# Kernel tuning notes

Hardware: AMD Instinct MI355X
Metric: run time of the kernel (lower is better)

The kernel has to match this reference:

```python
import jax, jax.numpy as jnp
import numpy as np

D = 768
H = 12
B, T = 2, 2048


def _layernorm(x, g, b, eps=1e-5):
    m = jnp.mean(x, axis=-1, keepdims=True)
    v = jnp.mean((x - m) ** 2, axis=-1, keepdims=True)
    return (x - m) * jax.lax.rsqrt(v + eps) * g + b


def setup_inputs() -> dict:
    key = jax.random.key(0)
    ks = jax.random.split(key, 10)
    s = 0.02
    return {
        "x": jax.random.normal(ks[0], (B, T, D), dtype=jnp.float32),
        "attn_mask": jnp.ones((B, T), dtype=jnp.int32),
        "Wq": jax.random.normal(ks[1], (D, D), dtype=jnp.float32) * s,
        "Wk": jax.random.normal(ks[2], (D, D), dtype=jnp.float32) * s,
        "Wv": jax.random.normal(ks[3], (D, D), dtype=jnp.float32) * s,
        "Wo": jax.random.normal(ks[4], (D, D), dtype=jnp.float32) * s,
        "bo": jnp.zeros((D,), dtype=jnp.float32),
        "ln1_g": jnp.ones((D,), dtype=jnp.float32),
        "ln1_b": jnp.zeros((D,), dtype=jnp.float32),
        "ln2_g": jnp.ones((D,), dtype=jnp.float32),
        "ln2_b": jnp.zeros((D,), dtype=jnp.float32),
        "W1": jax.random.normal(ks[5], (D, 4 * D), dtype=jnp.float32) * s,
        "b1": jnp.zeros((4 * D,), dtype=jnp.float32),
        "W2": jax.random.normal(ks[6], (4 * D, D), dtype=jnp.float32) * s,
        "b2": jnp.zeros((D,), dtype=jnp.float32),
    }


def reference(x, attn_mask, Wq, Wk, Wv, Wo, bo, ln1_g, ln1_b, ln2_g, ln2_b, W1, b1, W2, b2):
    d = x.shape[-1]
    hs = d // H
    # --- multi-head self-attention on ln1(x) ---
    h = _layernorm(x, ln1_g, ln1_b)
    q = jnp.einsum("btd,dhk->bhtk", h, Wq.reshape(d, H, hs))
    k = jnp.einsum("btd,dhk->bhtk", h, Wk.reshape(d, H, hs))
    v = jnp.einsum("btd,dhk->bhtk", h, Wv.reshape(d, H, hs))
    # NOTE: original scales by embed_dim**-0.5 (C = embed_dim), not head_size
    scores = jnp.einsum("bhtk,bhsk->bhts", q, k) * (d ** -0.5)
    key_mask = (attn_mask == 0)[:, None, None, :]  # [B,1,1,T] over key dim
    scores = jnp.where(key_mask, -jnp.inf, scores)
    wei = jax.nn.softmax(scores, axis=-1)
    out = jnp.einsum("bhts,bhsk->bhtk", wei, v)
    out = out.transpose(0, 2, 1, 3).reshape(x.shape)  # concat heads -> [B,T,D]
    x = x + out @ Wo + bo
    # --- feed-forward on ln2(x) ---
    h2 = _layernorm(x, ln2_g, ln2_b)
    ff = jax.nn.relu(h2 @ W1 + b1) @ W2 + b2
    return x + ff
```

## Files before the change

kernel.cpp:

```cpp
#include <hip/hip_runtime.h>
#include <hip/hip_bf16.h>


typedef unsigned short u16;
typedef unsigned int u32;
typedef __attribute__((ext_vector_type(8))) short s16x8;
typedef __attribute__((ext_vector_type(4))) short s16x4;
typedef __attribute__((ext_vector_type(4))) float fx4;

#define D_MODEL 768
#define NH 12
#define HS 64
#define TT 2048
#define BB 2

__device__ __forceinline__ u16 f2bf(float f) {
  union { float f; u32 u; } v; v.f = f;
  u32 r = v.u + 0x7fffu + ((v.u >> 16) & 1u);
  return (u16)(r >> 16);
}
__device__ __forceinline__ float bf2f(u16 h) {
  union { u32 u; float f; } v; v.u = ((u32)h) << 16; return v.f;
}
__device__ __forceinline__ s16x4 pack4(float a, float b, float c, float d) {
  union { __hip_bfloat162 h2[2]; s16x4 v; } u;
  u.h2[0] = __float22bfloat162_rn({a, b});
  u.h2[1] = __float22bfloat162_rn({c, d});
  return u.v;
}

__device__ __forceinline__ void async16(const void* g, void* l) {
  __builtin_amdgcn_global_load_lds(
      (const __attribute__((address_space(1))) u32*)g,
      (__attribute__((address_space(3))) u32*)l, 16, 0, 0);
}

__global__ __launch_bounds__(256) void preproc(
    const float* __restrict__ x, const int* __restrict__ mask,
    const float* __restrict__ Wq, const float* __restrict__ Wk,
    const float* __restrict__ Wv, const float* __restrict__ Wo,
    const float* __restrict__ W1, const float* __restrict__ W2,
    const float* __restrict__ g1, const float* __restrict__ be1,
    u16* __restrict__ WqkvT, u16* __restrict__ WoT,
    u16* __restrict__ W1T, u16* __restrict__ W2T,
    u16* __restrict__ h1, float* __restrict__ mb) {
  __shared__ float t[32][33];
  __shared__ float ss[4], ssq[4];
  const int bid = blockIdx.x, tid = threadIdx.x;
  if (bid < 6912) {
    const float* in; u16* out; int R, C, cx, cy;
    if (bid < 1728) {
      int wsel = bid / 576, s = bid % 576;
      in = wsel == 0 ? Wq : wsel == 1 ? Wk : Wv;
      out = WqkvT + (size_t)wsel * 768 * 768;
      R = 768; C = 768; cx = s % 24; cy = s / 24;
    } else if (bid < 2304) {
      int s = bid - 1728; in = Wo; out = WoT;
      R = 768; C = 768; cx = s % 24; cy = s / 24;
    } else if (bid < 4608) {
      int s = bid - 2304; in = W1; out = W1T;
      R = 768; C = 3072; cx = s % 96; cy = s / 96;
    } else {
      int s = bid - 4608; in = W2; out = W2T;
      R = 3072; C = 768; cx = s % 24; cy = s / 24;
    }
    int c0 = cx * 32, r0 = cy * 32, xx = tid & 31, yy = tid >> 5;
    for (int i = 0; i < 4; i++)
      t[yy + i * 8][xx] = in[(size_t)(r0 + yy + i * 8) * C + c0 + xx];
    __syncthreads();
    for (int i = 0; i < 4; i++)
      out[(size_t)(c0 + yy + i * 8) * R + r0 + xx] = f2bf(t[xx][yy + i * 8]);
  } else if (bid < 11008) {
    int row = bid - 6912;
    const float* xr = x + (size_t)row * D_MODEL;
    float v0 = xr[tid], v1 = xr[tid + 256], v2 = xr[tid + 512];
    float s = v0 + v1 + v2, sq = v0 * v0 + v1 * v1 + v2 * v2;
    for (int m = 1; m < 64; m <<= 1) { s += __shfl_xor(s, m); sq += __shfl_xor(sq, m); }
    int w = tid >> 6;
    if ((tid & 63) == 0) { ss[w] = s; ssq[w] = sq; }
    __syncthreads();
    s = ss[0] + ss[1] + ss[2] + ss[3];
    sq = ssq[0] + ssq[1] + ssq[2] + ssq[3];
    float mean = s * (1.f / D_MODEL);
    float var = sq * (1.f / D_MODEL) - mean * mean;
    float rstd = rsqrtf(var + 1e-5f);
    u16* orow = h1 + (size_t)row * D_MODEL;
    orow[tid]       = f2bf((v0 - mean) * rstd * g1[tid]       + be1[tid]);
    orow[tid + 256] = f2bf((v1 - mean) * rstd * g1[tid + 256] + be1[tid + 256]);
    orow[tid + 512] = f2bf((v2 - mean) * rstd * g1[tid + 512] + be1[tid + 512]);
  } else {
    int i = (bid - 11008) * 256 + tid;
    mb[i] = mask[i] ? 0.f : -1e30f;
  }
}

__global__ __launch_bounds__(256) void red_wo_ln(
    const u16* __restrict__ p0, const u16* __restrict__ p1,
    const u16* __restrict__ p2, const u16* __restrict__ p3,
    const float* __restrict__ x, const float* __restrict__ bo,
    const float* __restrict__ g, const float* __restrict__ be,
    float* __restrict__ yv, u16* __restrict__ h2) {
  int row = blockIdx.x, tid = threadIdx.x;
  size_t base = (size_t)row * D_MODEL;
  float v[3];
  float s = 0.f, sq = 0.f;
  for (int i = 0; i < 3; i++) {
    int c = tid + i * 256;
    size_t idx = base + c;
    float t = bf2f(p0[idx]) + bf2f(p1[idx]) + bf2f(p2[idx]) + bf2f(p3[idx])
            + x[idx] + bo[c];
    v[i] = t; yv[idx] = t;
    s += t; sq += t * t;
  }
  for (int m = 1; m < 64; m <<= 1) { s += __shfl_xor(s, m); sq += __shfl_xor(sq, m); }
  __shared__ float ss[4], ssq[4];
  int w = tid >> 6;
  if ((tid & 63) == 0) { ss[w] = s; ssq[w] = sq; }
  __syncthreads();
  s = ss[0] + ss[1] + ss[2] + ss[3];
  sq = ssq[0] + ssq[1] + ssq[2] + ssq[3];
  float mean = s * (1.f / D_MODEL);
  float var = sq * (1.f / D_MODEL) - mean * mean;
  float rstd = rsqrtf(var + 1e-5f);
  for (int i = 0; i < 3; i++) {
    int c = tid + i * 256;
    h2[base + c] = f2bf((v[i] - mean) * rstd * g[c] + be[c]);
  }
}

__global__ __launch_bounds__(256) void red_ff2(
    const u16* __restrict__ p0, const u16* __restrict__ p1,
    const u16* __restrict__ p2, const float* __restrict__ yv,
    const float* __restrict__ bias, float* __restrict__ out) {
  size_t i = ((size_t)blockIdx.x * 256 + threadIdx.x) * 4;
  int col = (int)(i % D_MODEL);
  ushort4 a = *(const ushort4*)(p0 + i);
  ushort4 b = *(const ushort4*)(p1 + i);
  ushort4 c = *(const ushort4*)(p2 + i);
  float4 y = *(const float4*)(yv + i);
  float4 o;
  o.x = bf2f(a.x) + bf2f(b.x) + bf2f(c.x) + y.x + bias[col];
  o.y = bf2f(a.y) + bf2f(b.y) + bf2f(c.y) + y.y + bias[col + 1];
  o.z = bf2f(a.z) + bf2f(b.z) + bf2f(c.z) + y.z + bias[col + 2];
  o.w = bf2f(a.w) + bf2f(b.w) + bf2f(c.w) + y.w + bias[col + 3];
  *(float4*)(out + i) = o;
}

template <int EPI>
__global__ __launch_bounds__(256) void gemm_bt(
    const u16* __restrict__ A, const u16* __restrict__ Bt,
    int M, int N, int K,
    u16* __restrict__ outb, const float* __restrict__ bias,
    float qs, u16* __restrict__ vtp,
    u16* __restrict__ p0, u16* __restrict__ p1,
    u16* __restrict__ p2, u16* __restrict__ p3) {
  __shared__ __align__(16) u16 lA[128 * 64];
  __shared__ __align__(16) u16 lB[128 * 64];
  const int tid = threadIdx.x;
  const int lane = tid & 63, w = tid >> 6;
  const int quad = lane >> 4, l15 = lane & 15;
  const int wm = w >> 1, wn = w & 1;
  const int bm = blockIdx.y, bn = blockIdx.x;
  const int Ksub = K / gridDim.z;
  const int k0 = blockIdx.z * Ksub;

  fx4 acc[4][4] = {};

  for (int kt = k0; kt < k0 + Ksub; kt += 64) {
    __syncthreads();
    #pragma unroll
    for (int t = 0; t < 4; t++) {
      int p = t * 256 + tid;
      int m = p >> 3, qp = p & 7, ql = qp ^ (m & 7);
      async16(A + (size_t)(bm * 128 + m) * K + kt + ql * 8,
              (char*)lA + t * 4096 + w * 1024);
    }
    #pragma unroll
    for (int t = 0; t < 4; t++) {
      int p = t * 256 + tid;
      int n = p >> 3, qp = p & 7, ql = qp ^ (n & 7);
      async16(Bt + (size_t)(bn * 128 + n) * K + kt + ql * 8,
              (char*)lB + t * 4096 + w * 1024);
    }
    __syncthreads();
    #pragma unroll
    for (int kk = 0; kk < 2; kk++) {
      s16x8 af[4], bfr[4];
      #pragma unroll
      for (int i = 0; i < 4; i++) {
        int m = wm * 64 + i * 16 + l15;
        af[i] = *(const s16x8*)((const char*)lA + m * 128 +
                                (((kk * 4 + quad) ^ (m & 7)) * 16));
      }
      #pragma unroll
      for (int j = 0; j < 4; j++) {
        int n = wn * 64 + j * 16 + l15;
        bfr[j] = *(const s16x8*)((const char*)lB + n * 128 +
                                 (((kk * 4 + quad) ^ (n & 7)) * 16));
      }
      #pragma unroll
      for (int i = 0; i < 4; i++)
        #pragma unroll
        for (int j = 0; j < 4; j++)
          acc[i][j] = __builtin_amdgcn_mfma_f32_16x16x32_bf16(af[i], bfr[j], acc[i][j], 0, 0, 0);
    }
  }

  u16* pb = nullptr;
  if (EPI == 3)
    pb = blockIdx.z == 0 ? p0 : blockIdx.z == 1 ? p1 : blockIdx.z == 2 ? p2 : p3;

  #pragma unroll
  for (int i = 0; i < 4; i++)
    #pragma unroll
    for (int j = 0; j < 4; j++) {
      int row0 = bm * 128 + wm * 64 + i * 16 + quad * 4;
      int col = bn * 128 + wn * 64 + j * 16 + l15;
      if (EPI == 0) {
        if (vtp != nullptr && col >= 1536) {
          int bb = row0 >> 11, t0 = row0 & 2047;
          ushort4 pk = {f2bf(acc[i][j][0]), f2bf(acc[i][j][1]),
                        f2bf(acc[i][j][2]), f2bf(acc[i][j][3])};
          *(ushort4*)(vtp + ((size_t)(bb * 768 + (col - 1536)) << 11) + t0) = pk;
        } else {
          float sc = (col < 768) ? qs : 1.f;
          for (int r = 0; r < 4; r++)
            outb[(size_t)(row0 + r) * N + col] = f2bf(acc[i][j][r] * sc);
        }
      } else if (EPI == 2) {
        for (int r = 0; r < 4; r++)
          outb[(size_t)(row0 + r) * N + col] = f2bf(fmaxf(acc[i][j][r] + bias[col], 0.f));
      } else {
        for (int r = 0; r < 4; r++)
          pb[(size_t)(row0 + r) * N + col] = f2bf(acc[i][j][r]);
      }
    }
}

__global__ __launch_bounds__(512) void attn_kernel(
    const u16* __restrict__ qkv, const u16* __restrict__ vt,
    const float* __restrict__ maskadd,
    u16* __restrict__ pO0, u16* __restrict__ pO1, float* __restrict__ pL) {
  __shared__ __align__(16) u16 sQ[128 * 64];
  __shared__ __align__(16) u16 sK[64 * 64];
  __shared__ __align__(16) u16 sV[64 * 68];
  __shared__ __align__(16) float smask[1024];
  const int bh = blockIdx.y, b = bh / NH, h = bh % NH;
  const int qt = blockIdx.x, sp = blockIdx.z;
  const int tid = threadIdx.x, lane = tid & 63, w = tid >> 6;
  const int quad = lane >> 4, l15 = lane & 15;

  for (int i = 0; i < 2; i++) {
    int p = i * 512 + tid;
    int m = p >> 3, qp = p & 7, ql = qp ^ (m & 7);
    async16(qkv + (size_t)(b * TT + qt * 128 + m) * 2304 + h * HS + ql * 8,
            (char*)sQ + i * 8192 + w * 1024);
  }
  smask[tid]       = maskadd[b * TT + sp * 1024 + tid];
  smask[tid + 512] = maskadd[b * TT + sp * 1024 + 512 + tid];
  const u16* vbase = vt + (size_t)bh * HS * TT + (size_t)(tid >> 3) * TT + sp * 1024;
  s16x8 vcur = *(const s16x8*)(vbase + (tid & 7) * 8);
  __syncthreads();

  const int qrow = w * 16 + l15;
  s16x8 aq0 = *(const s16x8*)((const char*)sQ + qrow * 128 + ((quad ^ (l15 & 7)) * 16));
  s16x8 aq1 = *(const s16x8*)((const char*)sQ + qrow * 128 + (((4 + quad) ^ (l15 & 7)) * 16));

  const char* pK0 = (const char*)sK + l15 * 128 + ((quad ^ (l15 & 7)) * 16);
  const char* pK1 = (const char*)sK + l15 * 128 + (((4 + quad) ^ (l15 & 7)) * 16);
  const char* pV  = (const char*)sV + l15 * 136 + quad * 8;
  char* vwr = (char*)sV + (tid >> 3) * 136 + (tid & 7) * 16;

  float lsum = 0.f;
  fx4 o[4] = {};

  for (int kc = 0; kc < 16; kc++) {
    __syncthreads();
    {
      int m = tid >> 3, qp = tid & 7, ql = qp ^ (m & 7);
      async16(qkv + (size_t)(b * TT + sp * 1024 + kc * 64 + m) * 2304 + D_MODEL + h * HS + ql * 8,
              (char*)sK + w * 1024);
    }
    *(s16x8*)vwr = vcur;
    __syncthreads();
    int kn = (kc < 15) ? (kc + 1) * 64 : kc * 64;
    s16x8 vnxt = *(const s16x8*)(vbase + kn + (tid & 7) * 8);

    #pragma unroll
    for (int kt = 0; kt < 4; kt++) {
      float4 mb = *(const float4*)&smask[kc * 64 + kt * 16 + quad * 4];
      fx4 s = {mb.x, mb.y, mb.z, mb.w};
      s16x8 ak0 = *(const s16x8*)(pK0 + kt * 2048);
      s16x8 ak1 = *(const s16x8*)(pK1 + kt * 2048);
      s = __builtin_amdgcn_mfma_f32_16x16x32_bf16(ak0, aq0, s, 0, 0, 0);
      s = __builtin_amdgcn_mfma_f32_16x16x32_bf16(ak1, aq1, s, 0, 0, 0);
      float e0 = __builtin_amdgcn_exp2f(s[0]);
      float e1 = __builtin_amdgcn_exp2f(s[1]);
      float e2 = __builtin_amdgcn_exp2f(s[2]);
      float e3 = __builtin_amdgcn_exp2f(s[3]);
      lsum += (e0 + e1) + (e2 + e3);
      s16x4 pB = pack4(e0, e1, e2, e3);
      #pragma unroll
      for (int jv = 0; jv < 4; jv++) {
        s16x4 av = *(const s16x4*)(pV + jv * 2176 + kt * 32);
        o[jv] = __builtin_amdgcn_mfma_f32_16x16x16bf16_1k(av, pB, o[jv], 0, 0, 0);
      }
    }
    vcur = vnxt;
  }

  lsum += __shfl_xor(lsum, 16);
  lsum += __shfl_xor(lsum, 32);

  const int tile = bh * 32 + qt * 2 + (w >> 2);
  const int sub = (w & 3) * 16;
  u16* po = sp ? pO1 : pO0;
  size_t base = (size_t)tile * 4096;
  for (int jv = 0; jv < 4; jv++)
    for (int r = 0; r < 4; r++) {
      int vd = jv * 16 + quad * 4 + r;
      po[base + vd * 64 + sub + l15] = f2bf(o[jv][r]);
    }
  if (quad == 0) pL[sp * 49152 + tile * 64 + sub + l15] = lsum;
}

__global__ __launch_bounds__(256) void attn_reduce(
    const u16* __restrict__ pO0, const u16* __restrict__ pO1,
    const float* __restrict__ pL, u16* __restrict__ out) {
  __shared__ float T[64 * 65];
  __shared__ float rinv[64];
  const int tile = blockIdx.x;
  const int bh = tile >> 5, qt = tile & 31, b = bh / NH, h = bh % NH;
  const int t = threadIdx.x;
  if (t < 64) rinv[t] = 1.f / (pL[tile * 64 + t] + pL[49152 + tile * 64 + t]);
  __syncthreads();
  size_t base = (size_t)tile * 4096;
  for (int i = 0; i < 16; i++) {
    int idx = i * 256 + t, vd = idx >> 6, q = idx & 63;
    T[vd * 65 + q] = (bf2f(pO0[base + idx]) + bf2f(pO1[base + idx])) * rinv[q];
  }
  __syncthreads();
  int q = t >> 2, vb = (t & 3) * 16;
  u16* orow = out + (size_t)(b * TT + qt * 64 + q) * D_MODEL + h * HS + vb;
  for (int i = 0; i < 8; i++) {
    int vd = vb + i * 2;
    u32 pk = (u32)f2bf(T[vd * 65 + q]) | ((u32)f2bf(T[(vd + 1) * 65 + q]) << 16);
    *(u32*)(orow + i * 2) = pk;
  }
}

extern "C" void kernel_launch(void* const* d_in, const int* in_sizes, int n_in,
                              void* d_out, int out_size, void* d_ws, size_t ws_size,
                              hipStream_t stream) {
  const float* x    = (const float*)d_in[0];
  const int*   mask = (const int*)d_in[1];
  const float* Wq   = (const float*)d_in[2];
  const float* Wk   = (const float*)d_in[3];
  const float* Wv   = (const float*)d_in[4];
  const float* Wo   = (const float*)d_in[5];
  const float* bo   = (const float*)d_in[6];
  const float* g1   = (const float*)d_in[7];
  const float* be1  = (const float*)d_in[8];
  const float* g2   = (const float*)d_in[9];
  const float* be2  = (const float*)d_in[10];
  const float* W1   = (const float*)d_in[11];
  const float* bb1  = (const float*)d_in[12];
  const float* W2   = (const float*)d_in[13];
  const float* bb2  = (const float*)d_in[14];
  float* out = (float*)d_out;
  char* ws = (char*)d_ws;

  u16*   WqkvT = (u16*)(ws + 0);
  u16*   WoT   = (u16*)(ws + 3538944);
  u16*   W1T   = (u16*)(ws + 4718592);
  u16*   W2T   = (u16*)(ws + 9437184);
  u16*   h1    = (u16*)(ws + 14155776);
  u16*   QKV   = (u16*)(ws + 20447232);
  u16*   Vt    = (u16*)(ws + 39321600);
  u16*   attn  = (u16*)(ws + 45613056);
  float* yv    = (float*)(ws + 51904512);
  float* mbias = yv;
  u16*   pO0   = h1;
  u16*   pO1   = (u16*)(ws + 51920896);
  float* pL    = (float*)(ws + 58212352);
  u16*   h2    = h1;
  u16*   ff1   = QKV;
  u16* pw0 = (u16*)(ws + 20447232);
  u16* pw1 = (u16*)(ws + 26738688);
  u16* pw2 = (u16*)(ws + 33030144);
  u16* pw3 = (u16*)(ws + 39321600);
  u16* pf0 = (u16*)(ws + 0);
  u16* pf1 = (u16*)(ws + 14155776);
  u16* pf2 = (u16*)(ws + 45613056);

  const float QS = 0.05205875399f;

  preproc<<<11024, 256, 0, stream>>>(x, mask, Wq, Wk, Wv, Wo, W1, W2,
                                     g1, be1, WqkvT, WoT, W1T, W2T, h1, mbias);
  gemm_bt<0><<<dim3(18, 32, 1), 256, 0, stream>>>(h1, WqkvT, 4096, 2304, 768,
      QKV, nullptr, QS, Vt, nullptr, nullptr, nullptr, nullptr);
  attn_kernel<<<dim3(16, 24, 2), 512, 0, stream>>>(QKV, Vt, mbias, pO0, pO1, pL);
  attn_reduce<<<768, 256, 0, stream>>>(pO0, pO1, pL, attn);
  gemm_bt<3><<<dim3(6, 32, 4), 256, 0, stream>>>(attn, WoT, 4096, 768, 768,
      nullptr, nullptr, 1.f, nullptr, pw0, pw1, pw2, pw3);
  red_wo_ln<<<4096, 256, 0, stream>>>(pw0, pw1, pw2, pw3, x, bo, g2, be2, yv, h2);
  gemm_bt<2><<<dim3(24, 32, 1), 256, 0, stream>>>(h2, W1T, 4096, 3072, 768,
      ff1, bb1, 1.f, nullptr, nullptr, nullptr, nullptr, nullptr);
  gemm_bt<3><<<dim3(6, 32, 3), 256, 0, stream>>>(ff1, W2T, 4096, 768, 3072,
      nullptr, nullptr, 1.f, nullptr, pf0, pf1, pf2, nullptr);
  red_ff2<<<3072, 256, 0, stream>>>(pf0, pf1, pf2, yv, bb2, out);
}
```

Measured before the change: 277.4 us.

## Shrink GEMM M-tile to 64, reduce split-K to 2, widen attention key chunks

The GEMM block tile drops from 128x128 to 64x128, doubling the grid along M. Split-K for the Wo and FF2 GEMMs falls to 2 partials, so the reduction kernels read fewer bf16 partial buffers. The attention kernel now stages 128 keys per iteration instead of 64, halving the loop trips and the barriers per key. The trade-offs are less operand reuse per GEMM block and more shared memory per attention block, which may lower occupancy.

```diff
diff --git a/kernel.cpp b/kernel.cpp
--- a/kernel.cpp
+++ b/kernel.cpp
@@ -96,7 +96,6 @@
 
 __global__ __launch_bounds__(256) void red_wo_ln(
     const u16* __restrict__ p0, const u16* __restrict__ p1,
-    const u16* __restrict__ p2, const u16* __restrict__ p3,
     const float* __restrict__ x, const float* __restrict__ bo,
     const float* __restrict__ g, const float* __restrict__ be,
     float* __restrict__ yv, u16* __restrict__ h2) {
@@ -107,8 +106,7 @@
   for (int i = 0; i < 3; i++) {
     int c = tid + i * 256;
     size_t idx = base + c;
-    float t = bf2f(p0[idx]) + bf2f(p1[idx]) + bf2f(p2[idx]) + bf2f(p3[idx])
-            + x[idx] + bo[c];
+    float t = bf2f(p0[idx]) + bf2f(p1[idx]) + x[idx] + bo[c];
     v[i] = t; yv[idx] = t;
     s += t; sq += t * t;
   }
@@ -130,19 +128,18 @@
 
 __global__ __launch_bounds__(256) void red_ff2(
     const u16* __restrict__ p0, const u16* __restrict__ p1,
-    const u16* __restrict__ p2, const float* __restrict__ yv,
+    const float* __restrict__ yv,
     const float* __restrict__ bias, float* __restrict__ out) {
   size_t i = ((size_t)blockIdx.x * 256 + threadIdx.x) * 4;
   int col = (int)(i % D_MODEL);
   ushort4 a = *(const ushort4*)(p0 + i);
   ushort4 b = *(const ushort4*)(p1 + i);
-  ushort4 c = *(const ushort4*)(p2 + i);
   float4 y = *(const float4*)(yv + i);
   float4 o;
-  o.x = bf2f(a.x) + bf2f(b.x) + bf2f(c.x) + y.x + bias[col];
-  o.y = bf2f(a.y) + bf2f(b.y) + bf2f(c.y) + y.y + bias[col + 1];
-  o.z = bf2f(a.z) + bf2f(b.z) + bf2f(c.z) + y.z + bias[col + 2];
-  o.w = bf2f(a.w) + bf2f(b.w) + bf2f(c.w) + y.w + bias[col + 3];
+  o.x = bf2f(a.x) + bf2f(b.x) + y.x + bias[col];
+  o.y = bf2f(a.y) + bf2f(b.y) + y.y + bias[col + 1];
+  o.z = bf2f(a.z) + bf2f(b.z) + y.z + bias[col + 2];
+  o.w = bf2f(a.w) + bf2f(b.w) + y.w + bias[col + 3];
   *(float4*)(out + i) = o;
 }
 
@@ -152,9 +149,8 @@
     int M, int N, int K,
     u16* __restrict__ outb, const float* __restrict__ bias,
     float qs, u16* __restrict__ vtp,
-    u16* __restrict__ p0, u16* __restrict__ p1,
-    u16* __restrict__ p2, u16* __restrict__ p3) {
-  __shared__ __align__(16) u16 lA[128 * 64];
+    u16* __restrict__ p0, u16* __restrict__ p1) {
+  __shared__ __align__(16) u16 lA[64 * 64];
   __shared__ __align__(16) u16 lB[128 * 64];
   const int tid = threadIdx.x;
   const int lane = tid & 63, w = tid >> 6;
@@ -164,15 +160,15 @@
   const int Ksub = K / gridDim.z;
   const int k0 = blockIdx.z * Ksub;
 
-  fx4 acc[4][4] = {};
+  fx4 acc[2][4] = {};
 
   for (int kt = k0; kt < k0 + Ksub; kt += 64) {
     __syncthreads();
     #pragma unroll
-    for (int t = 0; t < 4; t++) {
+    for (int t = 0; t < 2; t++) {
       int p = t * 256 + tid;
       int m = p >> 3, qp = p & 7, ql = qp ^ (m & 7);
-      async16(A + (size_t)(bm * 128 + m) * K + kt + ql * 8,
+      async16(A + (size_t)(bm * 64 + m) * K + kt + ql * 8,
               (char*)lA + t * 4096 + w * 1024);
     }
     #pragma unroll
@@ -185,10 +181,10 @@
     __syncthreads();
     #pragma unroll
     for (int kk = 0; kk < 2; kk++) {
-      s16x8 af[4], bfr[4];
+      s16x8 af[2], bfr[4];
       #pragma unroll
-      for (int i = 0; i < 4; i++) {
-        int m = wm * 64 + i * 16 + l15;
+      for (int i = 0; i < 2; i++) {
+        int m = wm * 32 + i * 16 + l15;
         af[i] = *(const s16x8*)((const char*)lA + m * 128 +
                                 (((kk * 4 + quad) ^ (m & 7)) * 16));
       }
@@ -199,22 +195,20 @@
                                  (((kk * 4 + quad) ^ (n & 7)) * 16));
       }
       #pragma unroll
-      for (int i = 0; i < 4; i++)
+      for (int i = 0; i < 2; i++)
         #pragma unroll
         for (int j = 0; j < 4; j++)
           acc[i][j] = __builtin_amdgcn_mfma_f32_16x16x32_bf16(af[i], bfr[j], acc[i][j], 0, 0, 0);
     }
   }
 
-  u16* pb = nullptr;
-  if (EPI == 3)
-    pb = blockIdx.z == 0 ? p0 : blockIdx.z == 1 ? p1 : blockIdx.z == 2 ? p2 : p3;
+  u16* pb = (EPI == 3) ? (blockIdx.z == 0 ? p0 : p1) : nullptr;
 
   #pragma unroll
-  for (int i = 0; i < 4; i++)
+  for (int i = 0; i < 2; i++)
     #pragma unroll
     for (int j = 0; j < 4; j++) {
-      int row0 = bm * 128 + wm * 64 + i * 16 + quad * 4;
+      int row0 = bm * 64 + wm * 32 + i * 16 + quad * 4;
       int col = bn * 128 + wn * 64 + j * 16 + l15;
       if (EPI == 0) {
         if (vtp != nullptr && col >= 1536) {
@@ -242,8 +236,8 @@
     const float* __restrict__ maskadd,
     u16* __restrict__ pO0, u16* __restrict__ pO1, float* __restrict__ pL) {
   __shared__ __align__(16) u16 sQ[128 * 64];
-  __shared__ __align__(16) u16 sK[64 * 64];
-  __shared__ __align__(16) u16 sV[64 * 68];
+  __shared__ __align__(16) u16 sK[128 * 64];
+  __shared__ __align__(16) u16 sV[64 * 132];
   __shared__ __align__(16) float smask[1024];
   const int bh = blockIdx.y, b = bh / NH, h = bh % NH;
   const int qt = blockIdx.x, sp = blockIdx.z;
@@ -259,7 +253,8 @@
   smask[tid]       = maskadd[b * TT + sp * 1024 + tid];
   smask[tid + 512] = maskadd[b * TT + sp * 1024 + 512 + tid];
   const u16* vbase = vt + (size_t)bh * HS * TT + (size_t)(tid >> 3) * TT + sp * 1024;
-  s16x8 vcur = *(const s16x8*)(vbase + (tid & 7) * 8);
+  s16x8 vc0 = *(const s16x8*)(vbase + (tid & 7) * 16);
+  s16x8 vc1 = *(const s16x8*)(vbase + (tid & 7) * 16 + 8);
   __syncthreads();
 
   const int qrow = w * 16 + l15;
@@ -268,27 +263,31 @@
 
   const char* pK0 = (const char*)sK + l15 * 128 + ((quad ^ (l15 & 7)) * 16);
   const char* pK1 = (const char*)sK + l15 * 128 + (((4 + quad) ^ (l15 & 7)) * 16);
-  const char* pV  = (const char*)sV + l15 * 136 + quad * 8;
-  char* vwr = (char*)sV + (tid >> 3) * 136 + (tid & 7) * 16;
+  const char* pV  = (const char*)sV + l15 * 264 + quad * 8;
+  char* vwr = (char*)sV + (tid >> 3) * 264 + (tid & 7) * 32;
 
   float lsum = 0.f;
   fx4 o[4] = {};
 
-  for (int kc = 0; kc < 16; kc++) {
-    __syncthreads();
-    {
-      int m = tid >> 3, qp = tid & 7, ql = qp ^ (m & 7);
-      async16(qkv + (size_t)(b * TT + sp * 1024 + kc * 64 + m) * 2304 + D_MODEL + h * HS + ql * 8,
-              (char*)sK + w * 1024);
-    }
-    *(s16x8*)vwr = vcur;
-    __syncthreads();
-    int kn = (kc < 15) ? (kc + 1) * 64 : kc * 64;
-    s16x8 vnxt = *(const s16x8*)(vbase + kn + (tid & 7) * 8);
-
-    #pragma unroll
-    for (int kt = 0; kt < 4; kt++) {
-      float4 mb = *(const float4*)&smask[kc * 64 + kt * 16 + quad * 4];
+  for (int kc = 0; kc < 8; kc++) {
+    __syncthreads();
+    #pragma unroll
+    for (int i = 0; i < 2; i++) {
+      int p = i * 512 + tid;
+      int m = p >> 3, qp = p & 7, ql = qp ^ (m & 7);
+      async16(qkv + (size_t)(b * TT + sp * 1024 + kc * 128 + m) * 2304 + D_MODEL + h * HS + ql * 8,
+              (char*)sK + i * 8192 + w * 1024);
+    }
+    *(s16x8*)vwr = vc0;
+    *(s16x8*)(vwr + 16) = vc1;
+    __syncthreads();
+    int kn = (kc < 7 ? kc + 1 : kc) * 128;
+    s16x8 vn0 = *(const s16x8*)(vbase + kn + (tid & 7) * 16);
+    s16x8 vn1 = *(const s16x8*)(vbase + kn + (tid & 7) * 16 + 8);
+
+    #pragma unroll
+    for (int kt = 0; kt < 8; kt++) {
+      float4 mb = *(const float4*)&smask[kc * 128 + kt * 16 + quad * 4];
       fx4 s = {mb.x, mb.y, mb.z, mb.w};
       s16x8 ak0 = *(const s16x8*)(pK0 + kt * 2048);
       s16x8 ak1 = *(const s16x8*)(pK1 + kt * 2048);
@@ -302,11 +301,11 @@
       s16x4 pB = pack4(e0, e1, e2, e3);
       #pragma unroll
       for (int jv = 0; jv < 4; jv++) {
-        s16x4 av = *(const s16x4*)(pV + jv * 2176 + kt * 32);
+        s16x4 av = *(const s16x4*)(pV + jv * 4224 + kt * 32);
         o[jv] = __builtin_amdgcn_mfma_f32_16x16x16bf16_1k(av, pB, o[jv], 0, 0, 0);
       }
     }
-    vcur = vnxt;
+    vc0 = vn0; vc1 = vn1;
   }
 
   lsum += __shfl_xor(lsum, 16);
@@ -387,26 +386,23 @@
   u16*   ff1   = QKV;
   u16* pw0 = (u16*)(ws + 20447232);
   u16* pw1 = (u16*)(ws + 26738688);
-  u16* pw2 = (u16*)(ws + 33030144);
-  u16* pw3 = (u16*)(ws + 39321600);
   u16* pf0 = (u16*)(ws + 0);
   u16* pf1 = (u16*)(ws + 14155776);
-  u16* pf2 = (u16*)(ws + 45613056);
 
   const float QS = 0.05205875399f;
 
   preproc<<<11024, 256, 0, stream>>>(x, mask, Wq, Wk, Wv, Wo, W1, W2,
                                      g1, be1, WqkvT, WoT, W1T, W2T, h1, mbias);
-  gemm_bt<0><<<dim3(18, 32, 1), 256, 0, stream>>>(h1, WqkvT, 4096, 2304, 768,
-      QKV, nullptr, QS, Vt, nullptr, nullptr, nullptr, nullptr);
+  gemm_bt<0><<<dim3(18, 64, 1), 256, 0, stream>>>(h1, WqkvT, 4096, 2304, 768,
+      QKV, nullptr, QS, Vt, nullptr, nullptr);
   attn_kernel<<<dim3(16, 24, 2), 512, 0, stream>>>(QKV, Vt, mbias, pO0, pO1, pL);
   attn_reduce<<<768, 256, 0, stream>>>(pO0, pO1, pL, attn);
-  gemm_bt<3><<<dim3(6, 32, 4), 256, 0, stream>>>(attn, WoT, 4096, 768, 768,
-      nullptr, nullptr, 1.f, nullptr, pw0, pw1, pw2, pw3);
-  red_wo_ln<<<4096, 256, 0, stream>>>(pw0, pw1, pw2, pw3, x, bo, g2, be2, yv, h2);
-  gemm_bt<2><<<dim3(24, 32, 1), 256, 0, stream>>>(h2, W1T, 4096, 3072, 768,
-      ff1, bb1, 1.f, nullptr, nullptr, nullptr, nullptr, nullptr);
-  gemm_bt<3><<<dim3(6, 32, 3), 256, 0, stream>>>(ff1, W2T, 4096, 768, 3072,
-      nullptr, nullptr, 1.f, nullptr, pf0, pf1, pf2, nullptr);
-  red_ff2<<<3072, 256, 0, stream>>>(pf0, pf1, pf2, yv, bb2, out);
-}
+  gemm_bt<3><<<dim3(6, 64, 2), 256, 0, stream>>>(attn, WoT, 4096, 768, 768,
+      nullptr, nullptr, 1.f, nullptr, pw0, pw1);
+  red_wo_ln<<<4096, 256, 0, stream>>>(pw0, pw1, x, bo, g2, be2, yv, h2);
+  gemm_bt<2><<<dim3(24, 64, 1), 256, 0, stream>>>(h2, W1T, 4096, 3072, 768,
+      ff1, bb1, 1.f, nullptr, nullptr, nullptr);
+  gemm_bt<3><<<dim3(6, 64, 2), 256, 0, stream>>>(ff1, W2T, 4096, 768, 3072,
+      nullptr, nullptr, 1.f, nullptr, pf0, pf1);
+  red_ff2<<<3072, 256, 0, stream>>>(pf0, pf1, yv, bb2, out);
+}
```

Measured after the change: 270.8 us. 2.4% less time.
